# Kernel tuning notes

Measured on AMD Instinct MI355X. Metric: run time of the kernel, lower is better.

Reference implementation:

```python
import jax, jax.numpy as jnp
import numpy as np

D = 512      # input_size
BR = 4       # branching factor (fan-in per internal node)
DEPTH = 8    # leaf level index; levels 0..DEPTH, root at level 0
N_NODES = (BR ** (DEPTH + 1) - 1) // (BR - 1)  # 87381


def setup_inputs() -> dict:
    key = jax.random.key(0)
    k1, k2, k3 = jax.random.split(key, 3)
    vectors = jax.random.normal(k1, (N_NODES, D), dtype=jnp.float32)
    scale = 1.0 / np.sqrt(D)
    wl = jax.random.normal(k2, (D, D), dtype=jnp.float32) * scale
    wr = jax.random.normal(k3, (D, D), dtype=jnp.float32) * scale
    return {"vectors": vectors, "wl": wl, "wr": wr, "branching": BR, "depth": DEPTH}


def reference(vectors, wl, wr, branching, depth):
    """Levelized CBTree forward over a complete `branching`-ary tree.

    vectors: [N, D] BFS-ordered node vectors (level l starts at (B^l-1)/(B-1)).
    Per node: h = tanh(x + sum_i lc_i * (h_i @ wl.T) + rc_i * (h_i @ wr.T)).
    """
    B, L = int(branching), int(depth)
    d = vectors.shape[-1]
    if B > 1:
        ind = jnp.arange(1, B + 1, dtype=vectors.dtype)  # 1-based child index
        lc = (B - ind) / (B - 1)
        rc = (ind - 1) / (B - 1)
    else:
        lc = jnp.full((1,), 0.5, dtype=vectors.dtype)
        rc = lc
    offsets = [(B ** l - 1) // (B - 1) for l in range(L + 1)]
    # leaves contribute their raw vectors (child.vector, no transform at leaf)
    h = vectors[offsets[L]: offsets[L] + B ** L]
    for l in range(L - 1, -1, -1):
        n = B ** l
        x = vectors[offsets[l]: offsets[l] + n]          # [n, D]
        hc = h.reshape(n, B, d)                           # children of level l
        tl = jnp.einsum('nbd,ed->nbe', hc, wl)            # wl(h_i) (Linear: h @ W.T)
        tr = jnp.einsum('nbd,ed->nbe', hc, wr)
        agg = jnp.einsum('b,nbe->ne', lc, tl) + jnp.einsum('b,nbe->ne', rc, tr)
        h = jnp.tanh(x + agg)                             # [n, D]
    return h  # [1, D] root hidden state
```

## Files before the change

kernel.cpp:

```cpp
#include <hip/hip_runtime.h>

typedef short short8 __attribute__((ext_vector_type(8)));
typedef float f32x4 __attribute__((ext_vector_type(4)));

#define D 512
#define KDIM 1024

static __device__ __forceinline__ unsigned short f2b(float f) {
    unsigned u = __builtin_bit_cast(unsigned, f);
    unsigned r = (u + 0x7fffu + ((u >> 16) & 1u)) >> 16;
    return (unsigned short)r;
}
static __device__ __forceinline__ float b2f(unsigned short u) {
    return __builtin_bit_cast(float, ((unsigned)u) << 16);
}
static __device__ __forceinline__ void split(float v, unsigned short& hi, unsigned short& lo) {
    hi = f2b(v);
    lo = f2b(v - b2f(hi));
}

static __device__ __forceinline__ void g2lds(const void* g, void* l) {
    __builtin_amdgcn_global_load_lds(
        (const __attribute__((address_space(1))) unsigned int*)g,
        (__attribute__((address_space(3))) unsigned int*)l, 16, 0, 0);
}

__global__ void pre_kernel(const float* __restrict__ leaves,
                           const float* __restrict__ wl, const float* __restrict__ wr,
                           unsigned short* __restrict__ Ah7,
                           unsigned short* __restrict__ Wh, unsigned short* __restrict__ Wl,
                           unsigned short* __restrict__ zbase) {
    int b = blockIdx.x;
    if (b < 4096) {
        int t = b * 256 + threadIdx.x;
        int p = t >> 6;
        int kc = (t & 63) << 3;
        const float c13 = 1.0f / 3.0f, c23 = 2.0f / 3.0f;
        const float* child = leaves;
        float4 a0 = *reinterpret_cast<const float4*>(child + (size_t)(4 * p + 0) * D + kc);
        float4 a1 = *reinterpret_cast<const float4*>(child + (size_t)(4 * p + 0) * D + kc + 4);
        float4 b0 = *reinterpret_cast<const float4*>(child + (size_t)(4 * p + 1) * D + kc);
        float4 b1 = *reinterpret_cast<const float4*>(child + (size_t)(4 * p + 1) * D + kc + 4);
        float4 c0 = *reinterpret_cast<const float4*>(child + (size_t)(4 * p + 2) * D + kc);
        float4 c1 = *reinterpret_cast<const float4*>(child + (size_t)(4 * p + 2) * D + kc + 4);
        float4 d0 = *reinterpret_cast<const float4*>(child + (size_t)(4 * p + 3) * D + kc);
        float4 d1 = *reinterpret_cast<const float4*>(child + (size_t)(4 * p + 3) * D + kc + 4);
        float ca[8] = {a0.x, a0.y, a0.z, a0.w, a1.x, a1.y, a1.z, a1.w};
        float cb[8] = {b0.x, b0.y, b0.z, b0.w, b1.x, b1.y, b1.z, b1.w};
        float cc[8] = {c0.x, c0.y, c0.z, c0.w, c1.x, c1.y, c1.z, c1.w};
        float cd[8] = {d0.x, d0.y, d0.z, d0.w, d1.x, d1.y, d1.z, d1.w};
        short8 uh, vh;
#pragma unroll
        for (int j = 0; j < 8; ++j) {
            float u = ca[j] + c23 * cb[j] + c13 * cc[j];
            float v = c13 * cb[j] + c23 * cc[j] + cd[j];
            uh[j] = (short)f2b(u);
            vh[j] = (short)f2b(v);
        }
        *reinterpret_cast<short8*>(&Ah7[(size_t)p * KDIM + kc]) = uh;
        *reinterpret_cast<short8*>(&Ah7[(size_t)p * KDIM + 512 + kc]) = vh;
    } else if (b < 6144) {
        int t = (b - 4096) * 256 + threadIdx.x;
        int e = t >> 10, k = t & 1023;
        float v = (k < 512) ? wl[e * 512 + k] : wr[e * 512 + (k - 512)];
        unsigned short h, l;
        split(v, h, l);
        Wh[t] = h; Wl[t] = l;
    } else {
        int t = (b - 6144) * 256 + threadIdx.x;
        *reinterpret_cast<short8*>(zbase + (size_t)t * 8) = (short8)0;
    }
}

template <int BM, bool ALO>
__global__ __launch_bounds__(256)
void gemm_tanh(const unsigned short* __restrict__ Ah, const unsigned short* __restrict__ Al,
               const unsigned short* __restrict__ Wh, const unsigned short* __restrict__ Wl,
               const float* __restrict__ x,
               unsigned short* __restrict__ nAh, unsigned short* __restrict__ nAl,
               int n) {
    constexpr int MF = (BM == 128) ? 4 : 2;
    constexpr int NF = 4;
    constexpr int APASS = BM / 32;
    __shared__ __align__(16) unsigned short Ahs[BM][64];
    __shared__ __align__(16) unsigned short Als[ALO ? BM : 1][64];
    __shared__ __align__(16) unsigned short Bhs[128][64];
    __shared__ __align__(16) unsigned short Bls[128][64];
    const int m0 = blockIdx.x * BM;
    const int e0 = blockIdx.y * 128;
    const int tid = threadIdx.x;
    const int lane = tid & 63, wid = tid >> 6;
    const int wr = (wid >> 1) * (BM / 2);
    const int wc = (wid & 1) * 64;

    f32x4 acc[MF][NF];
#pragma unroll
    for (int m = 0; m < MF; ++m)
#pragma unroll
        for (int nn = 0; nn < NF; ++nn) acc[m][nn] = (f32x4){0.f, 0.f, 0.f, 0.f};

    const int lrow = lane >> 3;
    const int lcol = (lane & 7) << 3;

    for (int kb = 0; kb < KDIM; kb += 64) {
#pragma unroll
        for (int p = 0; p < APASS; ++p) {
            int row = p * 32 + wid * 8;
            size_t g = (size_t)(m0 + row + lrow) * KDIM + kb + lcol;
            g2lds(&Ah[g], &Ahs[row][0]);
            if (ALO) g2lds(&Al[g], &Als[ALO ? row : 0][0]);
        }
#pragma unroll
        for (int p = 0; p < 4; ++p) {
            int row = p * 32 + wid * 8;
            size_t g = (size_t)(e0 + row + lrow) * KDIM + kb + lcol;
            g2lds(&Wh[g], &Bhs[row][0]);
            g2lds(&Wl[g], &Bls[row][0]);
        }
        __syncthreads();
#pragma unroll
        for (int kk = 0; kk < 64; kk += 32) {
            const int ka = kk + ((lane >> 4) << 3);
            short8 afh[MF], afl[MF], bfh[NF], bfl[NF];
#pragma unroll
            for (int m = 0; m < MF; ++m) {
                afh[m] = *reinterpret_cast<const short8*>(&Ahs[wr + m * 16 + (lane & 15)][ka]);
                if (ALO) afl[m] = *reinterpret_cast<const short8*>(&Als[ALO ? (wr + m * 16 + (lane & 15)) : 0][ka]);
            }
#pragma unroll
            for (int nn = 0; nn < NF; ++nn) {
                bfh[nn] = *reinterpret_cast<const short8*>(&Bhs[wc + nn * 16 + (lane & 15)][ka]);
                bfl[nn] = *reinterpret_cast<const short8*>(&Bls[wc + nn * 16 + (lane & 15)][ka]);
            }
#pragma unroll
            for (int m = 0; m < MF; ++m)
#pragma unroll
                for (int nn = 0; nn < NF; ++nn) {
                    acc[m][nn] = __builtin_amdgcn_mfma_f32_16x16x32_bf16(afh[m], bfh[nn], acc[m][nn], 0, 0, 0);
                    acc[m][nn] = __builtin_amdgcn_mfma_f32_16x16x32_bf16(afh[m], bfl[nn], acc[m][nn], 0, 0, 0);
                    if (ALO)
                        acc[m][nn] = __builtin_amdgcn_mfma_f32_16x16x32_bf16(afl[m], bfh[nn], acc[m][nn], 0, 0, 0);
                }
        }
        __syncthreads();
    }

    const int dr = (lane >> 4) << 2;
    const int dc = lane & 15;
    const float c13 = 1.0f / 3.0f, c23 = 2.0f / 3.0f;
#pragma unroll
    for (int m = 0; m < MF; ++m) {
        int rbase = m0 + wr + m * 16 + dr;
        if (rbase >= n) continue;
#pragma unroll
        for (int nn = 0; nn < NF; ++nn) {
            int col = e0 + wc + nn * 16 + dc;
            float hv[4];
#pragma unroll
            for (int j = 0; j < 4; ++j) {
                int row = rbase + j;
                hv[j] = (row < n) ? tanhf(acc[m][nn][j] + x[(size_t)row * D + col]) : 0.f;
            }
            int p = rbase >> 2;
            float u = hv[0] + c23 * hv[1] + c13 * hv[2];
            float v = c13 * hv[1] + c23 * hv[2] + hv[3];
            unsigned short h_, l_;
            split(u, h_, l_);
            nAh[(size_t)p * KDIM + col] = h_;
            nAl[(size_t)p * KDIM + col] = l_;
            split(v, h_, l_);
            nAh[(size_t)p * KDIM + 512 + col] = h_;
            nAl[(size_t)p * KDIM + 512 + col] = l_;
        }
    }
}

#define TBUF 6
template <bool FINAL>
__global__ __launch_bounds__(256)
void gemm_tiny(const unsigned short* __restrict__ Ah, const unsigned short* __restrict__ Al,
               const unsigned short* __restrict__ Wh, const unsigned short* __restrict__ Wl,
               const float* __restrict__ x,
               unsigned short* __restrict__ nAh, unsigned short* __restrict__ nAl,
               float* __restrict__ out, int n) {
    __shared__ __align__(16) unsigned short AhS[TBUF][32][64];
    __shared__ __align__(16) unsigned short AlS[TBUF][32][64];
    __shared__ __align__(16) unsigned short BhS[TBUF][64][64];
    __shared__ __align__(16) unsigned short BlS[TBUF][64][64];
    const int m0 = blockIdx.x * 32;
    const int e0 = blockIdx.y * 64;
    const int tid = threadIdx.x;
    const int lane = tid & 63, wid = tid >> 6;
    const int lrow = lane >> 3, lcol = (lane & 7) << 3;

    auto stage = [&](int s) {
        int slot = s % TBUF;
        int kb = s * 64;
        {
            int row = wid * 8;
            size_t g = (size_t)(m0 + row + lrow) * KDIM + kb + lcol;
            g2lds(&Ah[g], &AhS[slot][row][0]);
            g2lds(&Al[g], &AlS[slot][row][0]);
        }
#pragma unroll
        for (int p = 0; p < 2; ++p) {
            int row = wid * 16 + p * 8;
            size_t g = (size_t)(e0 + row + lrow) * KDIM + kb + lcol;
            g2lds(&Wh[g], &BhS[slot][row][0]);
            g2lds(&Wl[g], &BlS[slot][row][0]);
        }
    };

    f32x4 acc[2];
    acc[0] = (f32x4){0.f, 0.f, 0.f, 0.f};
    acc[1] = (f32x4){0.f, 0.f, 0.f, 0.f};

    stage(0); stage(1); stage(2); stage(3); stage(4);

#pragma unroll
    for (int t = 0; t < 16; ++t) {
        if (t <= 11)      { asm volatile("s_waitcnt vmcnt(24)" ::: "memory"); }
        else if (t == 12) { asm volatile("s_waitcnt vmcnt(18)" ::: "memory"); }
        else if (t == 13) { asm volatile("s_waitcnt vmcnt(12)" ::: "memory"); }
        else if (t == 14) { asm volatile("s_waitcnt vmcnt(6)"  ::: "memory"); }
        else              { asm volatile("s_waitcnt vmcnt(0)"  ::: "memory"); }
        __builtin_amdgcn_sched_barrier(0);
        __builtin_amdgcn_s_barrier();
        __builtin_amdgcn_sched_barrier(0);
        if (t + 5 < 16) stage(t + 5);
        const int slot = t % TBUF;
#pragma unroll
        for (int kk = 0; kk < 64; kk += 32) {
            const int ka = kk + ((lane >> 4) << 3);
            short8 afh[2], afl[2], bh, bl;
#pragma unroll
            for (int m = 0; m < 2; ++m) {
                afh[m] = *reinterpret_cast<const short8*>(&AhS[slot][m * 16 + (lane & 15)][ka]);
                afl[m] = *reinterpret_cast<const short8*>(&AlS[slot][m * 16 + (lane & 15)][ka]);
            }
            bh = *reinterpret_cast<const short8*>(&BhS[slot][wid * 16 + (lane & 15)][ka]);
            bl = *reinterpret_cast<const short8*>(&BlS[slot][wid * 16 + (lane & 15)][ka]);
#pragma unroll
            for (int m = 0; m < 2; ++m) {
                acc[m] = __builtin_amdgcn_mfma_f32_16x16x32_bf16(afh[m], bh, acc[m], 0, 0, 0);
                acc[m] = __builtin_amdgcn_mfma_f32_16x16x32_bf16(afh[m], bl, acc[m], 0, 0, 0);
                acc[m] = __builtin_amdgcn_mfma_f32_16x16x32_bf16(afl[m], bh, acc[m], 0, 0, 0);
            }
        }
    }

    const int dr = (lane >> 4) << 2;
    const int dc = lane & 15;
    const float c13 = 1.0f / 3.0f, c23 = 2.0f / 3.0f;
#pragma unroll
    for (int m = 0; m < 2; ++m) {
        int rbase = m0 + m * 16 + dr;
        if (rbase >= n) continue;
        int col = e0 + wid * 16 + dc;
        float hv[4];
#pragma unroll
        for (int j = 0; j < 4; ++j) {
            int row = rbase + j;
            hv[j] = (row < n) ? tanhf(acc[m][j] + x[(size_t)row * D + col]) : 0.f;
        }
        if (FINAL) {
            if (rbase == 0) out[col] = hv[0];
        } else {
            int p = rbase >> 2;
            float u = hv[0] + c23 * hv[1] + c13 * hv[2];
            float v = c13 * hv[1] + c23 * hv[2] + hv[3];
            unsigned short h_, l_;
            split(u, h_, l_);
            nAh[(size_t)p * KDIM + col] = h_;
            nAl[(size_t)p * KDIM + col] = l_;
            split(v, h_, l_);
            nAh[(size_t)p * KDIM + 512 + col] = h_;
            nAl[(size_t)p * KDIM + 512 + col] = l_;
        }
    }
}

extern "C" void kernel_launch(void* const* d_in, const int* in_sizes, int n_in,
                              void* d_out, int out_size, void* d_ws, size_t ws_size,
                              hipStream_t stream) {
    const float* vectors = (const float*)d_in[0];
    const float* wl = (const float*)d_in[1];
    const float* wr = (const float*)d_in[2];
    float* out = (float*)d_out;
    char* ws = (char*)d_ws;

    size_t cur = 0;
    auto alloc = [&](size_t bytes) -> char* {
        char* p = ws + cur;
        cur += (bytes + 255) & ~(size_t)255;
        return p;
    };
    unsigned short* Wh = (unsigned short*)alloc((size_t)512 * 1024 * 2);
    unsigned short* Wl = (unsigned short*)alloc((size_t)512 * 1024 * 2);
    const int arows[8] = {32, 32, 32, 64, 256, 1024, 4096, 16384};
    unsigned short *Ah[8], *Al[8];
    for (int l = 7; l >= 0; --l) {
        Ah[l] = (unsigned short*)alloc((size_t)arows[l] * KDIM * 2);
        Al[l] = (unsigned short*)alloc((size_t)arows[l] * KDIM * 2);
    }

    size_t off8 = 0;
    { size_t o = 0, c = 1; for (int l = 0; l <= 8; ++l) { if (l == 8) off8 = o; o += c; c *= 4; } }
    size_t off7 = off8 - 16384;

    pre_kernel<<<6240, 256, 0, stream>>>(vectors + off8 * (size_t)D, wl, wr,
                                         Ah[7], Wh, Wl, Ah[2]);

    gemm_tanh<128, false><<<dim3(128, 4), 256, 0, stream>>>(
        Ah[7], nullptr, Wh, Wl, vectors + off7 * (size_t)D, Ah[6], Al[6], 16384);

    gemm_tanh<64, true><<<dim3(64, 4), 256, 0, stream>>>(
        Ah[6], Al[6], Wh, Wl, vectors + (off7 - 4096) * (size_t)D, Ah[5], Al[5], 4096);

    const int xo[6] = {0, 1, 5, 21, 85, 341};
    for (int l = 5; l >= 1; --l) {
        int n = 1 << (2 * l);
        int gx = (n + 31) / 32;
        gemm_tiny<false><<<dim3(gx, 8), 256, 0, stream>>>(
            Ah[l], Al[l], Wh, Wl, vectors + (size_t)xo[l] * D,
            Ah[l - 1], Al[l - 1], nullptr, n);
    }
    gemm_tiny<true><<<dim3(1, 8), 256, 0, stream>>>(
        Ah[0], Al[0], Wh, Wl, vectors, nullptr, nullptr, out, 1);
}
```

Baseline: 209.3 us.

## Drop low-bf16 split terms in the two large GEMM levels and pipeline the mid-level GEMM

```diff
diff --git a/kernel.cpp b/kernel.cpp
--- a/kernel.cpp
+++ b/kernel.cpp
@@ -72,75 +72,50 @@
     }
 }
 
-template <int BM, bool ALO>
 __global__ __launch_bounds__(256)
-void gemm_tanh(const unsigned short* __restrict__ Ah, const unsigned short* __restrict__ Al,
-               const unsigned short* __restrict__ Wh, const unsigned short* __restrict__ Wl,
-               const float* __restrict__ x,
-               unsigned short* __restrict__ nAh, unsigned short* __restrict__ nAl,
-               int n) {
-    constexpr int MF = (BM == 128) ? 4 : 2;
-    constexpr int NF = 4;
-    constexpr int APASS = BM / 32;
-    __shared__ __align__(16) unsigned short Ahs[BM][64];
-    __shared__ __align__(16) unsigned short Als[ALO ? BM : 1][64];
+void gemm_l7(const unsigned short* __restrict__ Ah, const unsigned short* __restrict__ Wh,
+             const float* __restrict__ x, unsigned short* __restrict__ nAh, int n) {
+    __shared__ __align__(16) unsigned short Ahs[128][64];
     __shared__ __align__(16) unsigned short Bhs[128][64];
-    __shared__ __align__(16) unsigned short Bls[128][64];
-    const int m0 = blockIdx.x * BM;
+    const int m0 = blockIdx.x * 128;
     const int e0 = blockIdx.y * 128;
     const int tid = threadIdx.x;
     const int lane = tid & 63, wid = tid >> 6;
-    const int wr = (wid >> 1) * (BM / 2);
+    const int wr = (wid >> 1) * 64;
     const int wc = (wid & 1) * 64;
 
-    f32x4 acc[MF][NF];
-#pragma unroll
-    for (int m = 0; m < MF; ++m)
-#pragma unroll
-        for (int nn = 0; nn < NF; ++nn) acc[m][nn] = (f32x4){0.f, 0.f, 0.f, 0.f};
+    f32x4 acc[4][4];
+#pragma unroll
+    for (int m = 0; m < 4; ++m)
+#pragma unroll
+        for (int nn = 0; nn < 4; ++nn) acc[m][nn] = (f32x4){0.f, 0.f, 0.f, 0.f};
 
     const int lrow = lane >> 3;
     const int lcol = (lane & 7) << 3;
 
     for (int kb = 0; kb < KDIM; kb += 64) {
 #pragma unroll
-        for (int p = 0; p < APASS; ++p) {
-            int row = p * 32 + wid * 8;
-            size_t g = (size_t)(m0 + row + lrow) * KDIM + kb + lcol;
-            g2lds(&Ah[g], &Ahs[row][0]);
-            if (ALO) g2lds(&Al[g], &Als[ALO ? row : 0][0]);
-        }
-#pragma unroll
         for (int p = 0; p < 4; ++p) {
             int row = p * 32 + wid * 8;
-            size_t g = (size_t)(e0 + row + lrow) * KDIM + kb + lcol;
-            g2lds(&Wh[g], &Bhs[row][0]);
-            g2lds(&Wl[g], &Bls[row][0]);
+            g2lds(&Ah[(size_t)(m0 + row + lrow) * KDIM + kb + lcol], &Ahs[row][0]);
+            g2lds(&Wh[(size_t)(e0 + row + lrow) * KDIM + kb + lcol], &Bhs[row][0]);
         }
         __syncthreads();
 #pragma unroll
         for (int kk = 0; kk < 64; kk += 32) {
             const int ka = kk + ((lane >> 4) << 3);
-            short8 afh[MF], afl[MF], bfh[NF], bfl[NF];
-#pragma unroll
-            for (int m = 0; m < MF; ++m) {
-                afh[m] = *reinterpret_cast<const short8*>(&Ahs[wr + m * 16 + (lane & 15)][ka]);
-                if (ALO) afl[m] = *reinterpret_cast<const short8*>(&Als[ALO ? (wr + m * 16 + (lane & 15)) : 0][ka]);
-            }
-#pragma unroll
-            for (int nn = 0; nn < NF; ++nn) {
-                bfh[nn] = *reinterpret_cast<const short8*>(&Bhs[wc + nn * 16 + (lane & 15)][ka]);
-                bfl[nn] = *reinterpret_cast<const short8*>(&Bls[wc + nn * 16 + (lane & 15)][ka]);
-            }
-#pragma unroll
-            for (int m = 0; m < MF; ++m)
-#pragma unroll
-                for (int nn = 0; nn < NF; ++nn) {
-                    acc[m][nn] = __builtin_amdgcn_mfma_f32_16x16x32_bf16(afh[m], bfh[nn], acc[m][nn], 0, 0, 0);
-                    acc[m][nn] = __builtin_amdgcn_mfma_f32_16x16x32_bf16(afh[m], bfl[nn], acc[m][nn], 0, 0, 0);
-                    if (ALO)
-                        acc[m][nn] = __builtin_amdgcn_mfma_f32_16x16x32_bf16(afl[m], bfh[nn], acc[m][nn], 0, 0, 0);
-                }
+            short8 af[4], bf[4];
+#pragma unroll
+            for (int m = 0; m < 4; ++m)
+                af[m] = *reinterpret_cast<const short8*>(&Ahs[wr + m * 16 + (lane & 15)][ka]);
+#pragma unroll
+            for (int nn = 0; nn < 4; ++nn)
+                bf[nn] = *reinterpret_cast<const short8*>(&Bhs[wc + nn * 16 + (lane & 15)][ka]);
+#pragma unroll
+            for (int m = 0; m < 4; ++m)
+#pragma unroll
+                for (int nn = 0; nn < 4; ++nn)
+                    acc[m][nn] = __builtin_amdgcn_mfma_f32_16x16x32_bf16(af[m], bf[nn], acc[m][nn], 0, 0, 0);
         }
         __syncthreads();
     }
@@ -149,11 +124,102 @@
     const int dc = lane & 15;
     const float c13 = 1.0f / 3.0f, c23 = 2.0f / 3.0f;
 #pragma unroll
-    for (int m = 0; m < MF; ++m) {
+    for (int m = 0; m < 4; ++m) {
         int rbase = m0 + wr + m * 16 + dr;
         if (rbase >= n) continue;
 #pragma unroll
-        for (int nn = 0; nn < NF; ++nn) {
+        for (int nn = 0; nn < 4; ++nn) {
+            int col = e0 + wc + nn * 16 + dc;
+            float hv[4];
+#pragma unroll
+            for (int j = 0; j < 4; ++j) {
+                int row = rbase + j;
+                hv[j] = (row < n) ? tanhf(acc[m][nn][j] + x[(size_t)row * D + col]) : 0.f;
+            }
+            int p = rbase >> 2;
+            float u = hv[0] + c23 * hv[1] + c13 * hv[2];
+            float v = c13 * hv[1] + c23 * hv[2] + hv[3];
+            nAh[(size_t)p * KDIM + col] = f2b(u);
+            nAh[(size_t)p * KDIM + 512 + col] = f2b(v);
+        }
+    }
+}
+
+#define MBUF 4
+__global__ __launch_bounds__(256)
+void gemm_mid(const unsigned short* __restrict__ Ah, const unsigned short* __restrict__ Wh,
+              const float* __restrict__ x,
+              unsigned short* __restrict__ nAh, unsigned short* __restrict__ nAl, int n) {
+    __shared__ __align__(16) unsigned short AhS[MBUF][64][64];
+    __shared__ __align__(16) unsigned short BhS[MBUF][128][64];
+    const int m0 = blockIdx.x * 64;
+    const int e0 = blockIdx.y * 128;
+    const int tid = threadIdx.x;
+    const int lane = tid & 63, wid = tid >> 6;
+    const int wm = (wid >> 1) * 32;
+    const int wc = (wid & 1) * 64;
+    const int lrow = lane >> 3, lcol = (lane & 7) << 3;
+
+    auto stage = [&](int s) {
+        int slot = s & 3;
+        int kb = s * 64;
+#pragma unroll
+        for (int p = 0; p < 2; ++p) {
+            int row = wid * 16 + p * 8;
+            g2lds(&Ah[(size_t)(m0 + row + lrow) * KDIM + kb + lcol], &AhS[slot][row][0]);
+        }
+#pragma unroll
+        for (int p = 0; p < 4; ++p) {
+            int row = wid * 32 + p * 8;
+            g2lds(&Wh[(size_t)(e0 + row + lrow) * KDIM + kb + lcol], &BhS[slot][row][0]);
+        }
+    };
+
+    f32x4 acc[2][4];
+#pragma unroll
+    for (int m = 0; m < 2; ++m)
+#pragma unroll
+        for (int nn = 0; nn < 4; ++nn) acc[m][nn] = (f32x4){0.f, 0.f, 0.f, 0.f};
+
+    stage(0); stage(1); stage(2);
+
+#pragma unroll
+    for (int t = 0; t < 16; ++t) {
+        if (t <= 13)      { asm volatile("s_waitcnt vmcnt(12)" ::: "memory"); }
+        else if (t == 14) { asm volatile("s_waitcnt vmcnt(6)"  ::: "memory"); }
+        else              { asm volatile("s_waitcnt vmcnt(0)"  ::: "memory"); }
+        __builtin_amdgcn_sched_barrier(0);
+        __builtin_amdgcn_s_barrier();
+        __builtin_amdgcn_sched_barrier(0);
+        if (t + 3 < 16) stage(t + 3);
+        const int slot = t & 3;
+#pragma unroll
+        for (int kk = 0; kk < 64; kk += 32) {
+            const int ka = kk + ((lane >> 4) << 3);
+            short8 af[2], bf[4];
+#pragma unroll
+            for (int m = 0; m < 2; ++m)
+                af[m] = *reinterpret_cast<const short8*>(&AhS[slot][wm + m * 16 + (lane & 15)][ka]);
+#pragma unroll
+            for (int nn = 0; nn < 4; ++nn)
+                bf[nn] = *reinterpret_cast<const short8*>(&BhS[slot][wc + nn * 16 + (lane & 15)][ka]);
+#pragma unroll
+            for (int m = 0; m < 2; ++m)
+#pragma unroll
+                for (int nn = 0; nn < 4; ++nn)
+                    acc[m][nn] = __builtin_amdgcn_mfma_f32_16x16x32_bf16(af[m], bf[nn], acc[m][nn], 0, 0, 0);
+        }
+    }
+
+    const int dr = (lane >> 4) << 2;
+    const int dc = lane & 15;
+    const float c13 = 1.0f / 3.0f, c23 = 2.0f / 3.0f;
+#pragma unroll
+    for (int m = 0; m < 2; ++m) {
+        int rbase = m0 + wm + m * 16 + dr;
+        if (rbase >= n) continue;
+#pragma unroll
+        for (int nn = 0; nn < 4; ++nn) {
             int col = e0 + wc + nn * 16 + dc;
             float hv[4];
 #pragma unroll
@@ -311,11 +377,11 @@
     pre_kernel<<<6240, 256, 0, stream>>>(vectors + off8 * (size_t)D, wl, wr,
                                          Ah[7], Wh, Wl, Ah[2]);
 
-    gemm_tanh<128, false><<<dim3(128, 4), 256, 0, stream>>>(
-        Ah[7], nullptr, Wh, Wl, vectors + off7 * (size_t)D, Ah[6], Al[6], 16384);
-
-    gemm_tanh<64, true><<<dim3(64, 4), 256, 0, stream>>>(
-        Ah[6], Al[6], Wh, Wl, vectors + (off7 - 4096) * (size_t)D, Ah[5], Al[5], 4096);
+    gemm_l7<<<dim3(128, 4), 256, 0, stream>>>(
+        Ah[7], Wh, vectors + off7 * (size_t)D, Ah[6], 16384);
+
+    gemm_mid<<<dim3(64, 4), 256, 0, stream>>>(
+        Ah[6], Wh, vectors + (off7 - 4096) * (size_t)D, Ah[5], Al[5], 4096);
 
     const int xo[6] = {0, 1, 5, 21, 85, 341};
     for (int l = 5; l >= 1; --l) {
```

Measured after the change: 189.7 us (median of 2 runs). -9.4%, faster.
